# Kernel tuning notes

Hardware: AMD Instinct MI355X
Metric: run time of the kernel (lower is better)

Reference implementation:

```python
import jax, jax.numpy as jnp
import numpy as np
import math

IN_DIM = 2048
OUT_DIM = 2048
BATCH = 4096
BN_EPS = 1e-5


def setup_inputs() -> dict:
    key = jax.random.key(0)
    ks = jax.random.split(key, 6)
    x = jax.random.normal(ks[0], (BATCH, IN_DIM), dtype=jnp.float32)
    # scale ~ N(1.0, 0.1), translate = 0
    scale = 1.0 + 0.1 * jax.random.normal(ks[1], (1, IN_DIM), dtype=jnp.float32)
    translate = jnp.zeros((1, IN_DIM), dtype=jnp.float32)
    # kaiming-normal-ish init for wave_weight (fan_in), orthogonal-ish for base_weight
    wave_weight = jax.random.normal(ks[2], (OUT_DIM, IN_DIM), dtype=jnp.float32) * np.sqrt(2.0 / IN_DIM)
    bw = jax.random.normal(ks[3], (OUT_DIM, IN_DIM), dtype=jnp.float32)
    q, _ = jnp.linalg.qr(bw.T)  # (IN_DIM, OUT_DIM) orthonormal columns
    base_weight = q.T.astype(jnp.float32)
    gamma = jnp.ones((OUT_DIM,), dtype=jnp.float32)
    beta = jnp.zeros((OUT_DIM,), dtype=jnp.float32)
    return {"x": x, "scale": scale, "translate": translate,
            "wave_weight": wave_weight, "base_weight": base_weight,
            "gamma": gamma, "beta": beta}


def reference(x, scale, translate, wave_weight, base_weight, gamma, beta):
    # Bio wavelet: pi^-1/4 * cos(3u) * exp(-0.5 u^2), u = (x - t) / clamp(s, 1e-3)
    u = (x - translate) / jnp.maximum(scale, 1e-3)            # (B, in)
    wavelet = (math.pi ** -0.25) * jnp.cos(3.0 * u) * jnp.exp(-0.5 * u * u)
    # einsum 'boi,oi->bo' with singleton o broadcast == plain matmul
    wave_out = jnp.einsum('bi,oi->bo', wavelet, wave_weight)  # (B, out)
    base_out = jnp.einsum('bi,oi->bo', x, base_weight)        # (B, out)
    y = wave_out + 0.3 * base_out
    # BatchNorm1d (training mode: batch statistics, biased variance)
    mean = jnp.mean(y, axis=0)
    var = jnp.mean(jnp.square(y - mean), axis=0)
    out = gamma * (y - mean) * jax.lax.rsqrt(var + BN_EPS) + beta
    # dropout treated as identity (deterministic reference)
    return out
```

## Files before the change

kernel.cpp:

```cpp
#include <hip/hip_runtime.h>
#include <stdint.h>

#define IN_DIM 2048
#define OUT_DIM 2048
#define BATCH 4096
#define KDIM (2 * IN_DIM)
#define KROWB (KDIM * 2)
#define KH 2048
#define NTT 32
#define BN_EPS 1e-5f

typedef __attribute__((ext_vector_type(8))) short bf16x8;
typedef __attribute__((ext_vector_type(4))) float f32x4;

__device__ __forceinline__ unsigned short f2bf(float f) {
  union { float f; unsigned u; } v; v.f = f;
  unsigned r = v.u + 0x7FFFu + ((v.u >> 16) & 1u);
  return (unsigned short)(r >> 16);
}

__global__ void prep_act(const float* __restrict__ x,
                         const float* __restrict__ scale,
                         const float* __restrict__ translate,
                         unsigned short* __restrict__ A) {
  int e = (blockIdx.x * 256 + threadIdx.x) * 4;
  int b = e / IN_DIM;
  int i = e % IN_DIM;
  float4 xv = *(const float4*)(x + e);
  float4 sv = *(const float4*)(scale + i);
  float4 tv = *(const float4*)(translate + i);
  const float c = 0.7511255444649425f;
  float u0 = (xv.x - tv.x) / fmaxf(sv.x, 1e-3f);
  float u1 = (xv.y - tv.y) / fmaxf(sv.y, 1e-3f);
  float u2 = (xv.z - tv.z) / fmaxf(sv.z, 1e-3f);
  float u3 = (xv.w - tv.w) / fmaxf(sv.w, 1e-3f);
  ushort4 wv, xb;
  wv.x = f2bf(c * __cosf(3.0f * u0) * __expf(-0.5f * u0 * u0));
  wv.y = f2bf(c * __cosf(3.0f * u1) * __expf(-0.5f * u1 * u1));
  wv.z = f2bf(c * __cosf(3.0f * u2) * __expf(-0.5f * u2 * u2));
  wv.w = f2bf(c * __cosf(3.0f * u3) * __expf(-0.5f * u3 * u3));
  xb.x = f2bf(xv.x); xb.y = f2bf(xv.y); xb.z = f2bf(xv.z); xb.w = f2bf(xv.w);
  *(ushort4*)(A + (size_t)b * KDIM + i) = wv;
  *(ushort4*)(A + (size_t)b * KDIM + IN_DIM + i) = xb;
}

__global__ void prep_w(const float* __restrict__ ww,
                       const float* __restrict__ bw,
                       unsigned short* __restrict__ W) {
  int e = (blockIdx.x * 256 + threadIdx.x) * 4;
  int o = e / IN_DIM;
  int k = e % IN_DIM;
  float4 a = *(const float4*)(ww + e);
  float4 b = *(const float4*)(bw + e);
  ushort4 wa, wb;
  wa.x = f2bf(a.x); wa.y = f2bf(a.y); wa.z = f2bf(a.z); wa.w = f2bf(a.w);
  wb.x = f2bf(0.3f * b.x); wb.y = f2bf(0.3f * b.y);
  wb.z = f2bf(0.3f * b.z); wb.w = f2bf(0.3f * b.w);
  *(ushort4*)(W + (size_t)o * KDIM + k) = wa;
  *(ushort4*)(W + (size_t)o * KDIM + IN_DIM + k) = wb;
}


#define GLDS(gp, lo) __builtin_amdgcn_global_load_lds( \
    (const __attribute__((address_space(1))) void*)(gp), \
    (__attribute__((address_space(3))) void*)(lds + (lo) + ldsl), 16, 0, 0)

#define STG(u_, gp_, t_) do { \
  GLDS((gp_) + (size_t)(t_) * 128, (u_)); \
  GLDS((gp_) + (size_t)64 * KROWB + (size_t)(t_) * 128, (u_) + 8192); \
} while (0)

#define LDA4(mh, ss) do { \
  af[0] = *(const bf16x8*)(lds + P + rA + ((mh) * 4 + 0) * 2048 + (ss)); \
  af[1] = *(const bf16x8*)(lds + P + rA + ((mh) * 4 + 1) * 2048 + (ss)); \
  af[2] = *(const bf16x8*)(lds + P + rA + ((mh) * 4 + 2) * 2048 + (ss)); \
  af[3] = *(const bf16x8*)(lds + P + rA + ((mh) * 4 + 3) * 2048 + (ss)); \
} while (0)

#define LDB4(dst, ss) do { \
  dst[0] = *(const bf16x8*)(lds + P + rB + 0 * 2048 + (ss)); \
  dst[1] = *(const bf16x8*)(lds + P + rB + 1 * 2048 + (ss)); \
  dst[2] = *(const bf16x8*)(lds + P + rB + 2 * 2048 + (ss)); \
  dst[3] = *(const bf16x8*)(lds + P + rB + 3 * 2048 + (ss)); \
} while (0)

#define MM16(mh, bfr) do { \
  __builtin_amdgcn_s_setprio(1); \
  _Pragma("unroll") for (int i2 = 0; i2 < 4; ++i2) \
  _Pragma("unroll") for (int j2 = 0; j2 < 4; ++j2) \
    acc[(mh) * 4 + i2][j2] = __builtin_amdgcn_mfma_f32_16x16x32_bf16( \
        af[i2], bfr[j2], acc[(mh) * 4 + i2][j2], 0, 0, 0); \
  __builtin_amdgcn_s_setprio(0); \
} while (0)

#define LGKM0() asm volatile("s_waitcnt lgkmcnt(0)" ::: "memory")
#define VMW4()  asm volatile("s_waitcnt vmcnt(4)" ::: "memory")
#define VMW0()  asm volatile("s_waitcnt vmcnt(0)" ::: "memory")
#define BAR()   do { asm volatile("" ::: "memory"); __builtin_amdgcn_s_barrier(); \
                     asm volatile("" ::: "memory"); } while (0)

#define KTILE(u, DOST, DOST2, TAILB) do { \
  const int P = ((u) & 1) << 16; \
  const int Q = P ^ 65536; \
  LDA4(0, s0); LDB4(b0, s0); \
  if (DOST) STG(Q + 49152, bS1, (u) + 1); \
  BAR(); MM16(0, b0); LGKM0(); VMW4(); BAR(); \
  LDA4(1, s0); \
  if (DOST) STG(Q + 0, aS0, (u) + 1); \
  BAR(); MM16(1, b0); LGKM0(); BAR(); \
  LDA4(0, s1); LDB4(b1, s1); \
  if (DOST) STG(Q + 16384, aS1, (u) + 1); \
  BAR(); MM16(0, b1); LGKM0(); BAR(); \
  LDA4(1, s1); \
  if (DOST2) STG(P + 32768, bS0, (u) + 2); \
  BAR(); MM16(1, b1); LGKM0(); TAILB; BAR(); \
} while (0)

__global__ __launch_bounds__(512, 2) void gemm256(
    const unsigned short* __restrict__ A,
    const unsigned short* __restrict__ W,
    float* __restrict__ P0, float* __restrict__ P1) {
  __shared__ char lds[131072];
  const int tid = threadIdx.x;
  const int lane = tid & 63;
  const int wave = tid >> 6;
  const int wm = wave >> 2;
  const int wn = wave & 3;

  const int sw = ((blockIdx.x & 7) << 5) | (blockIdx.x >> 3);
  const int kz = sw >> 7;
  const int brow = ((sw >> 3) & 15) * 256;
  const int bcol = (sw & 7) * 256;
  const size_t kb = (size_t)kz * (KH * 2);

  const int srow = tid >> 3;
  const int gc16 = (tid & 7) ^ (srow & 7);
  const char* aS0 = (const char*)A + (size_t)(brow + srow) * KROWB + kb + gc16 * 16;
  const char* aS1 = aS0 + (size_t)128 * KROWB;
  const char* bS0 = (const char*)W + (size_t)(bcol + srow) * KROWB + kb + gc16 * 16;
  const char* bS1 = bS0 + (size_t)128 * KROWB;
  const int ldsl = wave * 1024;

  const int rA = (wm * 128 + (lane & 15)) * 128;
  const int rB = 32768 + (wn * 64 + (lane & 15)) * 128;
  const int s0 = (((lane >> 4)    ) ^ (lane & 7)) << 4;
  const int s1 = ((4 + (lane >> 4)) ^ (lane & 7)) << 4;

  f32x4 acc[8][4];
#pragma unroll
  for (int m = 0; m < 8; ++m)
#pragma unroll
    for (int n = 0; n < 4; ++n)
      acc[m][n] = (f32x4){0.f, 0.f, 0.f, 0.f};
  bf16x8 af[4], b0[4], b1[4];

  STG(32768, bS0, 0); STG(49152, bS1, 0); STG(0, aS0, 0); STG(16384, aS1, 0);
  STG(65536 + 32768, bS0, 1);
  VMW4(); BAR();

  for (int u = 0; u < NTT - 2; ++u)
    KTILE(u, 1, 1, VMW4());
  KTILE(NTT - 2, 1, 0, VMW0());
  KTILE(NTT - 1, 0, 0, VMW0());

  float* Pz = kz ? P1 : P0;
  const int r0 = brow + wm * 128 + (lane >> 4) * 4;
  const int c0 = bcol + wn * 64 + (lane & 15);
#pragma unroll
  for (int m = 0; m < 8; ++m)
#pragma unroll
    for (int n = 0; n < 4; ++n)
#pragma unroll
      for (int j = 0; j < 4; ++j)
        Pz[(size_t)(r0 + m * 16 + j) * OUT_DIM + (c0 + n * 16)] = acc[m][n][j];
}

__global__ void colstats2(const float* __restrict__ P1,
                          float* __restrict__ Y,
                          float* __restrict__ sums, float* __restrict__ sqs) {
  int col = (blockIdx.x & 7) * 256 + threadIdx.x;
  int r0 = (blockIdx.x >> 3) * 128;
  float s = 0.f, q = 0.f;
  for (int r = 0; r < 128; ++r) {
    size_t idx = (size_t)(r0 + r) * OUT_DIM + col;
    float v = Y[idx] + P1[idx];
    Y[idx] = v;
    s += v;
    q += v * v;
  }
  atomicAdd(&sums[col], s);
  atomicAdd(&sqs[col], q);
}

__global__ void bnorm(float* __restrict__ Y,
                      const float* __restrict__ sums, const float* __restrict__ sqs,
                      const float* __restrict__ gamma, const float* __restrict__ beta) {
  int e = (blockIdx.x * 256 + threadIdx.x) * 4;
  int c = e % OUT_DIM;
  float4 y = *(float4*)(Y + e);
  float4 s = *(const float4*)(sums + c);
  float4 q = *(const float4*)(sqs + c);
  float4 g = *(const float4*)(gamma + c);
  float4 bb = *(const float4*)(beta + c);
  const float invB = 1.0f / (float)BATCH;
  float m0 = s.x * invB, m1 = s.y * invB, m2 = s.z * invB, m3 = s.w * invB;
  float i0 = rsqrtf(q.x * invB - m0 * m0 + BN_EPS);
  float i1 = rsqrtf(q.y * invB - m1 * m1 + BN_EPS);
  float i2 = rsqrtf(q.z * invB - m2 * m2 + BN_EPS);
  float i3 = rsqrtf(q.w * invB - m3 * m3 + BN_EPS);
  y.x = g.x * (y.x - m0) * i0 + bb.x;
  y.y = g.y * (y.y - m1) * i1 + bb.y;
  y.z = g.z * (y.z - m2) * i2 + bb.z;
  y.w = g.w * (y.w - m3) * i3 + bb.w;
  *(float4*)(Y + e) = y;
}

extern "C" void kernel_launch(void* const* d_in, const int* in_sizes, int n_in,
                              void* d_out, int out_size, void* d_ws, size_t ws_size,
                              hipStream_t stream) {
  const float* x         = (const float*)d_in[0];
  const float* scale     = (const float*)d_in[1];
  const float* translate = (const float*)d_in[2];
  const float* ww        = (const float*)d_in[3];
  const float* bw        = (const float*)d_in[4];
  const float* gamma     = (const float*)d_in[5];
  const float* beta      = (const float*)d_in[6];
  float* out = (float*)d_out;

  char* ws = (char*)d_ws;
  unsigned short* A = (unsigned short*)ws;
  unsigned short* W = (unsigned short*)(ws + 33554432);
  float* P1   = (float*)(ws + 50331648);
  float* sums = (float*)(ws + 83886080);
  float* sqs  = sums + OUT_DIM;

  hipMemsetAsync(sums, 0, 2 * OUT_DIM * sizeof(float), stream);
  prep_act<<<(BATCH * IN_DIM) / 1024, 256, 0, stream>>>(x, scale, translate, A);
  prep_w<<<(OUT_DIM * IN_DIM) / 1024, 256, 0, stream>>>(ww, bw, W);
  gemm256<<<256, 512, 0, stream>>>(A, W, out, P1);
  colstats2<<<256, 256, 0, stream>>>(P1, out, sums, sqs);
  bnorm<<<(BATCH * OUT_DIM) / 1024, 256, 0, stream>>>(out, sums, sqs, gamma, beta);
}
```

Baseline: 122.5 us.

## Simplify GEMM prefetch to one-tile lookahead and defer split-K sum to bnorm

The GEMM main loop now issues all four global-to-LDS stages for the next k-tile at the start of each tile and waits with vmcnt(0) at the end. Previously bS0 was prefetched two tiles ahead and the other stages were interleaved with partial vmcnt(4) waits. This shortens prefetch distance and may expose more load latency. Separately, colstats no longer writes the summed split-K partial back to the output; bnorm re-reads both partials and adds them. That removes one full-matrix store at the cost of an extra read in bnorm.

```diff
diff --git a/kernel.cpp b/kernel.cpp
--- a/kernel.cpp
+++ b/kernel.cpp
@@ -94,26 +94,23 @@
 } while (0)
 
 #define LGKM0() asm volatile("s_waitcnt lgkmcnt(0)" ::: "memory")
-#define VMW4()  asm volatile("s_waitcnt vmcnt(4)" ::: "memory")
 #define VMW0()  asm volatile("s_waitcnt vmcnt(0)" ::: "memory")
 #define BAR()   do { asm volatile("" ::: "memory"); __builtin_amdgcn_s_barrier(); \
                      asm volatile("" ::: "memory"); } while (0)
 
-#define KTILE(u, DOST, DOST2, TAILB) do { \
+#define KTILE(u, DOST) do { \
   const int P = ((u) & 1) << 16; \
   const int Q = P ^ 65536; \
   LDA4(0, s0); LDB4(b0, s0); \
-  if (DOST) STG(Q + 49152, bS1, (u) + 1); \
-  BAR(); MM16(0, b0); LGKM0(); VMW4(); BAR(); \
+  if (DOST) { STG(Q + 32768, bS0, (u) + 1); STG(Q + 49152, bS1, (u) + 1); \
+              STG(Q + 0, aS0, (u) + 1); STG(Q + 16384, aS1, (u) + 1); } \
+  BAR(); MM16(0, b0); LGKM0(); BAR(); \
   LDA4(1, s0); \
-  if (DOST) STG(Q + 0, aS0, (u) + 1); \
   BAR(); MM16(1, b0); LGKM0(); BAR(); \
   LDA4(0, s1); LDB4(b1, s1); \
-  if (DOST) STG(Q + 16384, aS1, (u) + 1); \
   BAR(); MM16(0, b1); LGKM0(); BAR(); \
   LDA4(1, s1); \
-  if (DOST2) STG(P + 32768, bS0, (u) + 2); \
-  BAR(); MM16(1, b1); LGKM0(); TAILB; BAR(); \
+  BAR(); MM16(1, b1); LGKM0(); if (DOST) VMW0(); BAR(); \
 } while (0)
 
 __global__ __launch_bounds__(512, 2) void gemm256(
@@ -155,13 +152,11 @@
   bf16x8 af[4], b0[4], b1[4];
 
   STG(32768, bS0, 0); STG(49152, bS1, 0); STG(0, aS0, 0); STG(16384, aS1, 0);
-  STG(65536 + 32768, bS0, 1);
-  VMW4(); BAR();
-
-  for (int u = 0; u < NTT - 2; ++u)
-    KTILE(u, 1, 1, VMW4());
-  KTILE(NTT - 2, 1, 0, VMW0());
-  KTILE(NTT - 1, 0, 0, VMW0());
+  VMW0(); BAR();
+
+  for (int u = 0; u < NTT - 1; ++u)
+    KTILE(u, 1);
+  KTILE(NTT - 1, 0);
 
   float* Pz = kz ? P1 : P0;
   const int r0 = brow + wm * 128 + (lane >> 4) * 4;
@@ -175,16 +170,15 @@
         Pz[(size_t)(r0 + m * 16 + j) * OUT_DIM + (c0 + n * 16)] = acc[m][n][j];
 }
 
-__global__ void colstats2(const float* __restrict__ P1,
-                          float* __restrict__ Y,
+__global__ void colstats2(const float* __restrict__ P0,
+                          const float* __restrict__ P1,
                           float* __restrict__ sums, float* __restrict__ sqs) {
   int col = (blockIdx.x & 7) * 256 + threadIdx.x;
   int r0 = (blockIdx.x >> 3) * 128;
   float s = 0.f, q = 0.f;
   for (int r = 0; r < 128; ++r) {
     size_t idx = (size_t)(r0 + r) * OUT_DIM + col;
-    float v = Y[idx] + P1[idx];
-    Y[idx] = v;
+    float v = P0[idx] + P1[idx];
     s += v;
     q += v * v;
   }
@@ -192,12 +186,14 @@
   atomicAdd(&sqs[col], q);
 }
 
-__global__ void bnorm(float* __restrict__ Y,
-                      const float* __restrict__ sums, const float* __restrict__ sqs,
-                      const float* __restrict__ gamma, const float* __restrict__ beta) {
+__global__ void bnorm2(const float* __restrict__ P1, float* __restrict__ Y,
+                       const float* __restrict__ sums, const float* __restrict__ sqs,
+                       const float* __restrict__ gamma, const float* __restrict__ beta) {
   int e = (blockIdx.x * 256 + threadIdx.x) * 4;
   int c = e % OUT_DIM;
   float4 y = *(float4*)(Y + e);
+  float4 p = *(const float4*)(P1 + e);
+  y.x += p.x; y.y += p.y; y.z += p.z; y.w += p.w;
   float4 s = *(const float4*)(sums + c);
   float4 q = *(const float4*)(sqs + c);
   float4 g = *(const float4*)(gamma + c);
@@ -238,6 +234,6 @@
   prep_act<<<(BATCH * IN_DIM) / 1024, 256, 0, stream>>>(x, scale, translate, A);
   prep_w<<<(OUT_DIM * IN_DIM) / 1024, 256, 0, stream>>>(ww, bw, W);
   gemm256<<<256, 512, 0, stream>>>(A, W, out, P1);
-  colstats2<<<256, 256, 0, stream>>>(P1, out, sums, sqs);
-  bnorm<<<(BATCH * OUT_DIM) / 1024, 256, 0, stream>>>(out, sums, sqs, gamma, beta);
-}
+  colstats2<<<256, 256, 0, stream>>>(out, P1, sums, sqs);
+  bnorm2<<<(BATCH * OUT_DIM) / 1024, 256, 0, stream>>>(P1, out, sums, sqs, gamma, beta);
+}
```

Measured after the change: 125.3 us. 2.3% more time.
